# Optimization experiments

Hardware: AMD Instinct MI355X
Metric: run time of the kernel (lower is better)

Reference implementation:

```python
import jax, jax.numpy as jnp
import numpy as np
import math

DIM = 256

def setup_inputs() -> dict:
    key = jax.random.key(0)
    k1, k2, k3, k4, k5 = jax.random.split(key, 5)
    B, C, H, W = 4, DIM, 64, 64
    x = jax.random.normal(k1, (B, C, H, W), dtype=jnp.float32)
    fg_mask = jax.random.randint(k2, (B, 1, H, W), 0, 2, dtype=jnp.int32)
    s = 1.0 / math.sqrt(C)
    W_qkv = jax.random.uniform(k3, (3 * C, C), minval=-s, maxval=s, dtype=jnp.float32)
    W_proj = jax.random.uniform(k4, (C, C), minval=-s, maxval=s, dtype=jnp.float32)
    b_proj = jax.random.uniform(k5, (C,), minval=-s, maxval=s, dtype=jnp.float32)
    return {"x": x, "fg_mask": fg_mask, "W_qkv": W_qkv, "W_proj": W_proj, "b_proj": b_proj}

def reference(x, fg_mask, W_qkv, W_proj, b_proj):
    B, C, H, W = x.shape
    N = H * W
    xf = x.reshape(B, C, N).transpose(0, 2, 1)              # [B, N, C]
    qkv = jnp.einsum('bnc,dc->bnd', xf, W_qkv)              # [B, N, 3C]
    q, k, v = jnp.split(qkv, 3, axis=-1)                    # each [B, N, C]
    attn = jnp.einsum('bnc,bmc->bnm', q, k) / math.sqrt(C)  # [B, N, N]
    fg = fg_mask.reshape(B, N)                               # keys mask
    attn = jnp.where(fg[:, None, :] != 0, attn, -jnp.inf)
    a = jax.nn.softmax(attn, axis=-1)
    out = jnp.einsum('bnm,bmc->bnc', a, v)                  # [B, N, C]
    out = out @ W_proj.T + b_proj                           # [B, N, C]
    return out.transpose(0, 2, 1).reshape(B, C, H, W)
```

## Files before the change

### kernel.cpp

```cpp
#include <hip/hip_runtime.h>
#include <hip/hip_bf16.h>

#define BATCH 4
#define CDIM  256
#define NTOK  4096
#define THREE (3*CDIM)
#define VROWS 272

typedef unsigned short u16;
typedef unsigned char u8;
typedef long i64;
typedef __attribute__((ext_vector_type(4))) float f32x4;
typedef __attribute__((ext_vector_type(8))) short bf16x8;
typedef __attribute__((ext_vector_type(4))) unsigned int u32x4;

#define AS1 __attribute__((address_space(1)))
#define AS3 __attribute__((address_space(3)))

__device__ __forceinline__ u16 f2bf(float x) {
  unsigned int u = __float_as_uint(x);
  unsigned int r = (u + 0x7fffu + ((u >> 16) & 1u)) >> 16;
  return (u16)r;
}
__device__ __forceinline__ float bf2f(u16 v) {
  return __uint_as_float(((unsigned int)v) << 16);
}
__device__ __forceinline__ u8 f2fp8(float x) {
  int r = __builtin_amdgcn_cvt_pk_fp8_f32(x, 0.0f, 0, false);
  return (u8)(r & 0xff);
}
__device__ __forceinline__ void gload_lds16(const void* g, void* l) {
  __builtin_amdgcn_global_load_lds((AS1 const void*)g, (AS3 void*)l, 16, 0, 0);
}

#define SC8 0.30028132f

__global__ void k_prep(const float* __restrict__ Wqkv, const float* __restrict__ Wproj,
                       const int* __restrict__ fg,
                       u16* __restrict__ wq, u16* __restrict__ wp,
                       u16* __restrict__ Vt) {
  int i = blockIdx.x * 256 + threadIdx.x;
  const int nq = THREE * CDIM;
  const int np = CDIM * CDIM;
  const int nf = BATCH * NTOK;
  if (i < nq) { wq[i] = f2bf(Wqkv[i]); return; }
  int j = i - nq;
  if (j < np) { wp[j] = f2bf(Wproj[j]); return; }
  int k = j - np;
  if (k < nf) {
    int b = k >> 12, key = k & (NTOK - 1);
    Vt[((size_t)b * VROWS + 256) * NTOK + key] = fg[k] ? 0x3F80 : 0;
  }
}

__global__ __launch_bounds__(256) void k_transpose(const float* __restrict__ x, u16* __restrict__ xbf) {
  __shared__ float Ts[64][66];
  int n0 = blockIdx.x * 64;
  int c0 = blockIdx.y * 64;
  int b  = blockIdx.z;
  int tid = threadIdx.x;
  const float* xp = x + (size_t)b * CDIM * NTOK;
  int g16 = tid >> 4;
  int l16 = tid & 15;
#pragma unroll
  for (int i = 0; i < 4; ++i) {
    int cl = i * 16 + g16;
    int n4 = l16 * 4;
    *(f32x4*)&Ts[cl][n4] = *(const f32x4*)(xp + (size_t)(c0 + cl) * NTOK + n0 + n4);
  }
  __syncthreads();
#pragma unroll
  for (int i = 0; i < 4; ++i) {
    int nl = i * 16 + g16;
    int c4 = l16 * 4;
    ushort4 o;
    o.x = f2bf(Ts[c4 + 0][nl]);
    o.y = f2bf(Ts[c4 + 1][nl]);
    o.z = f2bf(Ts[c4 + 2][nl]);
    o.w = f2bf(Ts[c4 + 3][nl]);
    *(ushort4*)&xbf[((size_t)b * NTOK + n0 + nl) * CDIM + c0 + c4] = o;
  }
}

__global__ __launch_bounds__(256) void k_qkv(const u16* __restrict__ xbf, const u16* __restrict__ wq,
                                             const int* __restrict__ fg,
                                             u8* __restrict__ Qm8, u8* __restrict__ Km8,
                                             u16* __restrict__ Vt) {
  __shared__ u16 Al[128 * 64];
  __shared__ u16 Bl[128 * 64];
  int n0 = blockIdx.x * 128;
  int d0 = blockIdx.y * 128;
  int b  = blockIdx.z;
  int tid = threadIdx.x;
  int lane = tid & 63, w = tid >> 6;
  int lo = lane & 15, hi = lane >> 4;
  int wm = w >> 1, wn = w & 1;
  f32x4 acc[4][4] = {};
  const u16* Ab = xbf + ((size_t)b * NTOK + n0) * CDIM;
  const u16* Bb = wq + (size_t)d0 * CDIM;
  for (int kc = 0; kc < 256; kc += 64) {
    __syncthreads();
#pragma unroll
    for (int j = 0; j < 4; ++j) {
      int id = (j * 4 + w) * 64 + lane;
      int row = id >> 3, c = id & 7;
      int sc = c ^ (row & 7);
      gload_lds16(Ab + (size_t)row * CDIM + kc + sc * 8, &Al[(size_t)id * 8]);
      gload_lds16(Bb + (size_t)row * CDIM + kc + sc * 8, &Bl[(size_t)id * 8]);
    }
    __syncthreads();
#pragma unroll
    for (int kk = 0; kk < 2; ++kk) {
      bf16x8 af[4], bfr[4];
#pragma unroll
      for (int mi = 0; mi < 4; ++mi) {
        int row = wm * 64 + mi * 16 + lo;
        af[mi] = *(const bf16x8*)&Al[row * 64 + (((kk * 4 + hi) ^ (row & 7)) * 8)];
      }
#pragma unroll
      for (int ni = 0; ni < 4; ++ni) {
        int row = wn * 64 + ni * 16 + lo;
        bfr[ni] = *(const bf16x8*)&Bl[row * 64 + (((kk * 4 + hi) ^ (row & 7)) * 8)];
      }
#pragma unroll
      for (int mi = 0; mi < 4; ++mi)
#pragma unroll
        for (int ni = 0; ni < 4; ++ni)
          acc[mi][ni] = __builtin_amdgcn_mfma_f32_16x16x32_bf16(af[mi], bfr[ni], acc[mi][ni], 0, 0, 0);
    }
  }
  int seg = d0 >> 8;
#pragma unroll
  for (int mi = 0; mi < 4; ++mi) {
    int nbase = n0 + wm * 64 + mi * 16 + hi * 4;
#pragma unroll
    for (int ni = 0; ni < 4; ++ni) {
      int d = d0 + wn * 64 + ni * 16 + lo;
      if (seg == 0) {
#pragma unroll
        for (int r = 0; r < 4; ++r)
          Qm8[((size_t)b * NTOK + nbase + r) * CDIM + d] = f2fp8(acc[mi][ni][r] * SC8);
      } else if (seg == 1) {
        int dk = d - 256;
#pragma unroll
        for (int r = 0; r < 4; ++r)
          Km8[((size_t)b * NTOK + nbase + r) * CDIM + dk] = f2fp8(acc[mi][ni][r] * SC8);
      } else {
        int dv = d - 512;
        ushort4 pk;
        pk.x = fg[b * NTOK + nbase + 0] ? f2bf(acc[mi][ni][0]) : (u16)0;
        pk.y = fg[b * NTOK + nbase + 1] ? f2bf(acc[mi][ni][1]) : (u16)0;
        pk.z = fg[b * NTOK + nbase + 2] ? f2bf(acc[mi][ni][2]) : (u16)0;
        pk.w = fg[b * NTOK + nbase + 3] ? f2bf(acc[mi][ni][3]) : (u16)0;
        *(ushort4*)&Vt[((size_t)b * VROWS + dv) * NTOK + nbase] = pk;
      }
    }
  }
}

__global__ __launch_bounds__(256, 2) void k_attn(const u8* __restrict__ Qm8, const u8* __restrict__ Km8,
                                                 const u16* __restrict__ Vt,
                                                 u16* __restrict__ pacc, float2* __restrict__ pml,
                                                 int lsplit) {
  __shared__ u8  Kl[2][32 * 256];
  __shared__ u16 Vl[2][256 * 32];
  __shared__ u16 fgl[1024];
  const float FM = 12.0f;
  int nwg = gridDim.x;
  int cpx = nwg >> 3;
  int orig = blockIdx.x;
  int wg = (orig & 7) * cpx + (orig >> 3);
  int qt = wg & 31;
  int bs = wg >> 5;
  int s_k = bs & ((1 << lsplit) - 1);
  int b   = bs >> lsplit;
  int chunk = NTOK >> lsplit;
  int koff  = s_k * chunk;
  int iters = chunk >> 5;

  int tid = threadIdx.x;
  int lane = tid & 63, w = tid >> 6;
  int lo = lane & 15, hi = lane >> 4;
  int n0 = qt * 128 + w * 32;
  i64 qf[2][8];
#pragma unroll
  for (int s = 0; s < 2; ++s) {
    const u8* qp = Qm8 + ((size_t)b * NTOK + n0 + s * 16 + lo) * CDIM + hi * 8;
#pragma unroll
    for (int ks = 0; ks < 8; ++ks) qf[s][ks] = *(const i64*)(qp + ks * 32);
  }
  f32x4 acc[2][16] = {};
  float lsum[2] = {0.0f, 0.0f};
  const u8*  kbase = Km8 + (size_t)b * NTOK * CDIM;
  const u16* vbase = Vt + (size_t)b * VROWS * NTOK;
  const u16* fgrow = vbase + (size_t)256 * NTOK;
  int vr  = lane >> 2;
  int vc  = lane & 3;
  int srcA = lo + ((hi & 1) << 5);
  int srcB = srcA + 16;

  auto stage = [&](int buf, int m0) {
#pragma unroll
    for (int j = 0; j < 2; ++j) {
      int rl = w * 8 + j * 4 + (lane >> 4);
      int sb = ((lane & 15) << 4) ^ ((rl & 7) << 4);
      gload_lds16(kbase + (size_t)(m0 + rl) * CDIM + sb,
                  &Kl[buf][w * 2048 + j * 1024]);
    }
#pragma unroll
    for (int j = 0; j < 4; ++j) {
      int idx = j * 4 + w;
      int r = idx * 16 + vr;
      int d = vc ^ (r & 3) ^ ((r >> 2) & 3);
      gload_lds16(vbase + (size_t)r * NTOK + m0 + d * 8, &Vl[buf][idx * 512]);
    }
  };

  if (w < 2) gload_lds16(fgrow + koff + w * 512 + lane * 8, &fgl[w * 512 + lane * 8]);
  stage(0, koff);
  __syncthreads();
  for (int it = 0; it < iters; ++it) {
    int cur = it & 1;
    int m0 = koff + it * 32;
    if (it + 1 < iters) stage(cur ^ 1, m0 + 32);
    f32x4 sv[2][2];
#pragma unroll
    for (int s = 0; s < 2; ++s)
#pragma unroll
      for (int ni = 0; ni < 2; ++ni)
#pragma unroll
        for (int r = 0; r < 4; ++r) sv[s][ni][r] = -FM;
    __builtin_amdgcn_s_setprio(1);
#pragma unroll
    for (int ks = 0; ks < 8; ++ks) {
      i64 kf[2];
#pragma unroll
      for (int ni = 0; ni < 2; ++ni) {
        int row = ni * 16 + lo;
        int byteoff = row * 256 + ((((ks * 2 + (hi >> 1)) << 4) ^ ((row & 7) << 4))) + ((hi & 1) << 3);
        kf[ni] = *(const i64*)((const char*)&Kl[cur][0] + byteoff);
      }
#pragma unroll
      for (int s = 0; s < 2; ++s)
#pragma unroll
        for (int ni = 0; ni < 2; ++ni)
          sv[s][ni] = __builtin_amdgcn_mfma_f32_16x16x32_fp8_fp8(kf[ni], qf[s][ks], sv[s][ni], 0, 0, 0);
    }
    __builtin_amdgcn_s_setprio(0);
    float p0[2][2][4];
#pragma unroll
    for (int ni = 0; ni < 2; ++ni) {
      ushort4 fgu = *(const ushort4*)&fgl[it * 32 + ni * 16 + hi * 4];
      float fg0 = bf2f(fgu.x), fg1 = bf2f(fgu.y), fg2 = bf2f(fgu.z), fg3 = bf2f(fgu.w);
#pragma unroll
      for (int s = 0; s < 2; ++s) {
        float e0 = exp2f(sv[s][ni][0]);
        float e1 = exp2f(sv[s][ni][1]);
        float e2 = exp2f(sv[s][ni][2]);
        float e3 = exp2f(sv[s][ni][3]);
        lsum[s] += e0 * fg0 + e1 * fg1 + e2 * fg2 + e3 * fg3;
        p0[s][ni][0] = e0; p0[s][ni][1] = e1; p0[s][ni][2] = e2; p0[s][ni][3] = e3;
      }
    }
    bf16x8 pbf[2];
#pragma unroll
    for (int s = 0; s < 2; ++s) {
      unsigned int pk00, pk01, pk10, pk11;
      asm("v_cvt_pk_bf16_f32 %0, %1, %2" : "=v"(pk00) : "v"(p0[s][0][0]), "v"(p0[s][0][1]));
      asm("v_cvt_pk_bf16_f32 %0, %1, %2" : "=v"(pk01) : "v"(p0[s][0][2]), "v"(p0[s][0][3]));
      asm("v_cvt_pk_bf16_f32 %0, %1, %2" : "=v"(pk10) : "v"(p0[s][1][0]), "v"(p0[s][1][1]));
      asm("v_cvt_pk_bf16_f32 %0, %1, %2" : "=v"(pk11) : "v"(p0[s][1][2]), "v"(p0[s][1][3]));
      int a00 = __shfl((int)pk00, srcA); int a10 = __shfl((int)pk10, srcA);
      int a01 = __shfl((int)pk01, srcA); int a11 = __shfl((int)pk11, srcA);
      int b00 = __shfl((int)pk00, srcB); int b10 = __shfl((int)pk10, srcB);
      int b01 = __shfl((int)pk01, srcB); int b11 = __shfl((int)pk11, srcB);
      u32x4 tv;
      tv.x = (unsigned)(hi < 2 ? a00 : a10);
      tv.y = (unsigned)(hi < 2 ? a01 : a11);
      tv.z = (unsigned)(hi < 2 ? b00 : b10);
      tv.w = (unsigned)(hi < 2 ? b01 : b11);
      pbf[s] = __builtin_bit_cast(bf16x8, tv);
    }
    __builtin_amdgcn_s_setprio(1);
#pragma unroll
    for (int cf = 0; cf < 16; ++cf) {
      int row = cf * 16 + lo;
      const char* vp = (const char*)&Vl[cur][0] + row * 64 + ((hi ^ (lo & 3) ^ ((lo >> 2) & 3)) << 4);
      bf16x8 vb = *(const bf16x8*)vp;
#pragma unroll
      for (int s = 0; s < 2; ++s)
        acc[s][cf] = __builtin_amdgcn_mfma_f32_16x16x32_bf16(vb, pbf[s], acc[s][cf], 0, 0, 0);
    }
    __builtin_amdgcn_s_setprio(0);
    __syncthreads();
  }
  float ls[2];
#pragma unroll
  for (int s = 0; s < 2; ++s) {
    float t = lsum[s];
    t += __shfl_xor(t, 16);
    t += __shfl_xor(t, 32);
    ls[s] = t;
  }
  u16* pb = pacc + (((size_t)s_k * BATCH + b) * NTOK + n0) * CDIM;
  float2* pm = pml + ((size_t)s_k * BATCH + b) * NTOK + n0;
#pragma unroll
  for (int s = 0; s < 2; ++s) {
#pragma unroll
    for (int cf = 0; cf < 16; ++cf) {
      ushort4 st;
      st.x = f2bf(acc[s][cf][0]);
      st.y = f2bf(acc[s][cf][1]);
      st.z = f2bf(acc[s][cf][2]);
      st.w = f2bf(acc[s][cf][3]);
      *(ushort4*)&pb[(size_t)(s * 16 + lo) * CDIM + cf * 16 + hi * 4] = st;
    }
    if (lane < 16) {
      float2 v; v.x = FM; v.y = ls[s];
      pm[s * 16 + lane] = v;
    }
  }
}

__global__ __launch_bounds__(256) void k_proj(const u16* __restrict__ pacc,
                                              const float2* __restrict__ pml,
                                              const u16* __restrict__ wp,
                                              const float* __restrict__ bproj, float* __restrict__ out) {
  __shared__ u16 Al[128 * 64];
  __shared__ u16 Bl[128][72];
  __shared__ float invl[128];
  const size_t RN = (size_t)BATCH * NTOK;
  int n0 = blockIdx.x * 128;
  int c0 = blockIdx.y * 128;
  int b  = blockIdx.z;
  int tid = threadIdx.x;
  int lane = tid & 63, w = tid >> 6;
  int lo = lane & 15, hi = lane >> 4;
  int wm = w >> 1, wn = w & 1;
  if (tid < 128) {
    float d = 0.0f;
#pragma unroll
    for (int s = 0; s < 4; ++s)
      d += pml[(size_t)s * RN + (size_t)b * NTOK + n0 + tid].y;
    invl[tid] = 1.0f / d;
  }
  f32x4 acc[4][4] = {};
  const u16* Ab = wp + (size_t)c0 * CDIM;
  for (int kcs = 0; kcs < 256; kcs += 64) {
    __syncthreads();
#pragma unroll
    for (int j = 0; j < 4; ++j) {
      int id = (j * 4 + w) * 64 + lane;
      int row = id >> 3, c = id & 7;
      int sc = c ^ (row & 7);
      gload_lds16(Ab + (size_t)row * CDIM + kcs + sc * 8, &Al[(size_t)id * 8]);
    }
#pragma unroll
    for (int i = 0; i < 4; ++i) {
      int cid = i * 256 + tid;
      int row = cid >> 3, cc = cid & 7;
      size_t off = ((size_t)b * NTOK + n0 + row) * CDIM + kcs + cc * 8;
      float v[8] = {0, 0, 0, 0, 0, 0, 0, 0};
#pragma unroll
      for (int s = 0; s < 4; ++s) {
        uint4 u = *(const uint4*)(pacc + (size_t)s * RN * CDIM + off);
        const u16* pu = (const u16*)&u;
#pragma unroll
        for (int j = 0; j < 8; ++j) v[j] += bf2f(pu[j]);
      }
      float iv = invl[row];
      ushort4 o0, o1;
      o0.x = f2bf(v[0] * iv); o0.y = f2bf(v[1] * iv); o0.z = f2bf(v[2] * iv); o0.w = f2bf(v[3] * iv);
      o1.x = f2bf(v[4] * iv); o1.y = f2bf(v[5] * iv); o1.z = f2bf(v[6] * iv); o1.w = f2bf(v[7] * iv);
      *(ushort4*)&Bl[row][cc * 8]     = o0;
      *(ushort4*)&Bl[row][cc * 8 + 4] = o1;
    }
    __syncthreads();
#pragma unroll
    for (int kk = 0; kk < 2; ++kk) {
      bf16x8 af[4], bfr[4];
#pragma unroll
      for (int mi = 0; mi < 4; ++mi) {
        int row = wm * 64 + mi * 16 + lo;
        af[mi] = *(const bf16x8*)&Al[row * 64 + (((kk * 4 + hi) ^ (row & 7)) * 8)];
      }
#pragma unroll
      for (int ni = 0; ni < 4; ++ni) bfr[ni] = *(const bf16x8*)&Bl[wn * 64 + ni * 16 + lo][kk * 32 + hi * 8];
#pragma unroll
      for (int mi = 0; mi < 4; ++mi)
#pragma unroll
        for (int ni = 0; ni < 4; ++ni)
          acc[mi][ni] = __builtin_amdgcn_mfma_f32_16x16x32_bf16(af[mi], bfr[ni], acc[mi][ni], 0, 0, 0);
    }
  }
#pragma unroll
  for (int mi = 0; mi < 4; ++mi) {
    int cbase = c0 + wm * 64 + mi * 16 + hi * 4;
#pragma unroll
    for (int r = 0; r < 4; ++r) {
      float bias = bproj[cbase + r];
#pragma unroll
      for (int ni = 0; ni < 4; ++ni) {
        int n = n0 + wn * 64 + ni * 16 + lo;
        out[((size_t)b * CDIM + cbase + r) * NTOK + n] = acc[mi][ni][r] + bias;
      }
    }
  }
}

extern "C" void kernel_launch(void* const* d_in, const int* in_sizes, int n_in,
                              void* d_out, int out_size, void* d_ws, size_t ws_size,
                              hipStream_t stream) {
  const float* x     = (const float*)d_in[0];
  const int*   fg    = (const int*)d_in[1];
  const float* Wqkv  = (const float*)d_in[2];
  const float* Wproj = (const float*)d_in[3];
  const float* bproj = (const float*)d_in[4];
  float* out = (float*)d_out;
  char* ws = (char*)d_ws;
  u16*   xbf  = (u16*)(ws);
  u8*    Qm8  = (u8*)(ws + 8388608);
  u8*    Km8  = (u8*)(ws + 12582912);
  u16*   Vt   = (u16*)(ws + 16777216);
  u16*   wq   = (u16*)(ws + 25690112);
  u16*   wp   = (u16*)(ws + 26083328);
  u16*   pacc = (u16*)(ws + 26214400);
  float2* pml = (float2*)(ws + 59768832);

  k_prep<<<1088, 256, 0, stream>>>(Wqkv, Wproj, fg, wq, wp, Vt);
  k_transpose<<<dim3(64, 4, 4), 256, 0, stream>>>(x, xbf);
  k_qkv<<<dim3(32, 6, 4), 256, 0, stream>>>(xbf, wq, fg, Qm8, Km8, Vt);
  k_attn<<<512, 256, 0, stream>>>(Qm8, Km8, Vt, pacc, pml, 2);
  k_proj<<<dim3(32, 2, 4), 256, 0, stream>>>(pacc, pml, wp, bproj, out);
}
```

Before: 138.6 us.

## Halve attention query tile per wave to double workgroups and raise occupancy

Each wave in the attention kernel now handles 16 query rows instead of 32, so a workgroup covers 64 queries and the grid doubles to 1024 workgroups. Launch bounds go to 3 waves per SIMD, which fits because the accumulator register footprint is halved. The goal is more parallelism and better latency hiding across CUs. In exchange, every K/V tile staged into LDS is reused by half as many queries, so K/V traffic and LDS staging per unit of work double.

```diff
diff --git a/kernel.cpp b/kernel.cpp
--- a/kernel.cpp
+++ b/kernel.cpp
@@ -158,7 +158,7 @@
   }
 }
 
-__global__ __launch_bounds__(256, 2) void k_attn(const u8* __restrict__ Qm8, const u8* __restrict__ Km8,
+__global__ __launch_bounds__(256, 3) void k_attn(const u8* __restrict__ Qm8, const u8* __restrict__ Km8,
                                                  const u16* __restrict__ Vt,
                                                  u16* __restrict__ pacc, float2* __restrict__ pml,
                                                  int lsplit) {
@@ -170,8 +170,8 @@
   int cpx = nwg >> 3;
   int orig = blockIdx.x;
   int wg = (orig & 7) * cpx + (orig >> 3);
-  int qt = wg & 31;
-  int bs = wg >> 5;
+  int qt = wg & 63;
+  int bs = wg >> 6;
   int s_k = bs & ((1 << lsplit) - 1);
   int b   = bs >> lsplit;
   int chunk = NTOK >> lsplit;
@@ -181,16 +181,13 @@
   int tid = threadIdx.x;
   int lane = tid & 63, w = tid >> 6;
   int lo = lane & 15, hi = lane >> 4;
-  int n0 = qt * 128 + w * 32;
-  i64 qf[2][8];
-#pragma unroll
-  for (int s = 0; s < 2; ++s) {
-    const u8* qp = Qm8 + ((size_t)b * NTOK + n0 + s * 16 + lo) * CDIM + hi * 8;
-#pragma unroll
-    for (int ks = 0; ks < 8; ++ks) qf[s][ks] = *(const i64*)(qp + ks * 32);
-  }
-  f32x4 acc[2][16] = {};
-  float lsum[2] = {0.0f, 0.0f};
+  int n0 = qt * 64 + w * 16;
+  i64 qf[8];
+  const u8* qp = Qm8 + ((size_t)b * NTOK + n0 + lo) * CDIM + hi * 8;
+#pragma unroll
+  for (int ks = 0; ks < 8; ++ks) qf[ks] = *(const i64*)(qp + ks * 32);
+  f32x4 acc[16] = {};
+  float lsum = 0.0f;
   const u8*  kbase = Km8 + (size_t)b * NTOK * CDIM;
   const u16* vbase = Vt + (size_t)b * VROWS * NTOK;
   const u16* fgrow = vbase + (size_t)256 * NTOK;
@@ -223,13 +220,11 @@
     int cur = it & 1;
     int m0 = koff + it * 32;
     if (it + 1 < iters) stage(cur ^ 1, m0 + 32);
-    f32x4 sv[2][2];
-#pragma unroll
-    for (int s = 0; s < 2; ++s)
-#pragma unroll
-      for (int ni = 0; ni < 2; ++ni)
-#pragma unroll
-        for (int r = 0; r < 4; ++r) sv[s][ni][r] = -FM;
+    f32x4 sv[2];
+#pragma unroll
+    for (int ni = 0; ni < 2; ++ni)
+#pragma unroll
+      for (int r = 0; r < 4; ++r) sv[ni][r] = -FM;
     __builtin_amdgcn_s_setprio(1);
 #pragma unroll
     for (int ks = 0; ks < 8; ++ks) {
@@ -241,35 +236,28 @@
         kf[ni] = *(const i64*)((const char*)&Kl[cur][0] + byteoff);
       }
 #pragma unroll
-      for (int s = 0; s < 2; ++s)
-#pragma unroll
-        for (int ni = 0; ni < 2; ++ni)
-          sv[s][ni] = __builtin_amdgcn_mfma_f32_16x16x32_fp8_fp8(kf[ni], qf[s][ks], sv[s][ni], 0, 0, 0);
+      for (int ni = 0; ni < 2; ++ni)
+        sv[ni] = __builtin_amdgcn_mfma_f32_16x16x32_fp8_fp8(kf[ni], qf[ks], sv[ni], 0, 0, 0);
     }
     __builtin_amdgcn_s_setprio(0);
-    float p0[2][2][4];
+    float p0[2][4];
 #pragma unroll
     for (int ni = 0; ni < 2; ++ni) {
       ushort4 fgu = *(const ushort4*)&fgl[it * 32 + ni * 16 + hi * 4];
-      float fg0 = bf2f(fgu.x), fg1 = bf2f(fgu.y), fg2 = bf2f(fgu.z), fg3 = bf2f(fgu.w);
-#pragma unroll
-      for (int s = 0; s < 2; ++s) {
-        float e0 = exp2f(sv[s][ni][0]);
-        float e1 = exp2f(sv[s][ni][1]);
-        float e2 = exp2f(sv[s][ni][2]);
-        float e3 = exp2f(sv[s][ni][3]);
-        lsum[s] += e0 * fg0 + e1 * fg1 + e2 * fg2 + e3 * fg3;
-        p0[s][ni][0] = e0; p0[s][ni][1] = e1; p0[s][ni][2] = e2; p0[s][ni][3] = e3;
-      }
-    }
-    bf16x8 pbf[2];
-#pragma unroll
-    for (int s = 0; s < 2; ++s) {
+      float e0 = exp2f(sv[ni][0]);
+      float e1 = exp2f(sv[ni][1]);
+      float e2 = exp2f(sv[ni][2]);
+      float e3 = exp2f(sv[ni][3]);
+      lsum += e0 * bf2f(fgu.x) + e1 * bf2f(fgu.y) + e2 * bf2f(fgu.z) + e3 * bf2f(fgu.w);
+      p0[ni][0] = e0; p0[ni][1] = e1; p0[ni][2] = e2; p0[ni][3] = e3;
+    }
+    bf16x8 pbf;
+    {
       unsigned int pk00, pk01, pk10, pk11;
-      asm("v_cvt_pk_bf16_f32 %0, %1, %2" : "=v"(pk00) : "v"(p0[s][0][0]), "v"(p0[s][0][1]));
-      asm("v_cvt_pk_bf16_f32 %0, %1, %2" : "=v"(pk01) : "v"(p0[s][0][2]), "v"(p0[s][0][3]));
-      asm("v_cvt_pk_bf16_f32 %0, %1, %2" : "=v"(pk10) : "v"(p0[s][1][0]), "v"(p0[s][1][1]));
-      asm("v_cvt_pk_bf16_f32 %0, %1, %2" : "=v"(pk11) : "v"(p0[s][1][2]), "v"(p0[s][1][3]));
+      asm("v_cvt_pk_bf16_f32 %0, %1, %2" : "=v"(pk00) : "v"(p0[0][0]), "v"(p0[0][1]));
+      asm("v_cvt_pk_bf16_f32 %0, %1, %2" : "=v"(pk01) : "v"(p0[0][2]), "v"(p0[0][3]));
+      asm("v_cvt_pk_bf16_f32 %0, %1, %2" : "=v"(pk10) : "v"(p0[1][0]), "v"(p0[1][1]));
+      asm("v_cvt_pk_bf16_f32 %0, %1, %2" : "=v"(pk11) : "v"(p0[1][2]), "v"(p0[1][3]));
       int a00 = __shfl((int)pk00, srcA); int a10 = __shfl((int)pk10, srcA);
       int a01 = __shfl((int)pk01, srcA); int a11 = __shfl((int)pk11, srcA);
       int b00 = __shfl((int)pk00, srcB); int b10 = __shfl((int)pk10, srcB);
@@ -279,7 +267,7 @@
       tv.y = (unsigned)(hi < 2 ? a01 : a11);
       tv.z = (unsigned)(hi < 2 ? b00 : b10);
       tv.w = (unsigned)(hi < 2 ? b01 : b11);
-      pbf[s] = __builtin_bit_cast(bf16x8, tv);
+      pbf = __builtin_bit_cast(bf16x8, tv);
     }
     __builtin_amdgcn_s_setprio(1);
 #pragma unroll
@@ -287,38 +275,32 @@
       int row = cf * 16 + lo;
       const char* vp = (const char*)&Vl[cur][0] + row * 64 + ((hi ^ (lo & 3) ^ ((lo >> 2) & 3)) << 4);
       bf16x8 vb = *(const bf16x8*)vp;
-#pragma unroll
-      for (int s = 0; s < 2; ++s)
-        acc[s][cf] = __builtin_amdgcn_mfma_f32_16x16x32_bf16(vb, pbf[s], acc[s][cf], 0, 0, 0);
+      acc[cf] = __builtin_amdgcn_mfma_f32_16x16x32_bf16(vb, pbf, acc[cf], 0, 0, 0);
     }
     __builtin_amdgcn_s_setprio(0);
     __syncthreads();
   }
-  float ls[2];
-#pragma unroll
-  for (int s = 0; s < 2; ++s) {
-    float t = lsum[s];
+  float ls;
+  {
+    float t = lsum;
     t += __shfl_xor(t, 16);
     t += __shfl_xor(t, 32);
-    ls[s] = t;
+    ls = t;
   }
   u16* pb = pacc + (((size_t)s_k * BATCH + b) * NTOK + n0) * CDIM;
   float2* pm = pml + ((size_t)s_k * BATCH + b) * NTOK + n0;
 #pragma unroll
-  for (int s = 0; s < 2; ++s) {
-#pragma unroll
-    for (int cf = 0; cf < 16; ++cf) {
-      ushort4 st;
-      st.x = f2bf(acc[s][cf][0]);
-      st.y = f2bf(acc[s][cf][1]);
-      st.z = f2bf(acc[s][cf][2]);
-      st.w = f2bf(acc[s][cf][3]);
-      *(ushort4*)&pb[(size_t)(s * 16 + lo) * CDIM + cf * 16 + hi * 4] = st;
-    }
-    if (lane < 16) {
-      float2 v; v.x = FM; v.y = ls[s];
-      pm[s * 16 + lane] = v;
-    }
+  for (int cf = 0; cf < 16; ++cf) {
+    ushort4 st;
+    st.x = f2bf(acc[cf][0]);
+    st.y = f2bf(acc[cf][1]);
+    st.z = f2bf(acc[cf][2]);
+    st.w = f2bf(acc[cf][3]);
+    *(ushort4*)&pb[(size_t)lo * CDIM + cf * 16 + hi * 4] = st;
+  }
+  if (lane < 16) {
+    float2 v; v.x = FM; v.y = ls;
+    pm[lane] = v;
   }
 }
 
@@ -430,6 +412,6 @@
   k_prep<<<1088, 256, 0, stream>>>(Wqkv, Wproj, fg, wq, wp, Vt);
   k_transpose<<<dim3(64, 4, 4), 256, 0, stream>>>(x, xbf);
   k_qkv<<<dim3(32, 6, 4), 256, 0, stream>>>(xbf, wq, fg, Qm8, Km8, Vt);
-  k_attn<<<512, 256, 0, stream>>>(Qm8, Km8, Vt, pacc, pml, 2);
+  k_attn<<<1024, 256, 0, stream>>>(Qm8, Km8, Vt, pacc, pml, 2);
   k_proj<<<dim3(32, 2, 4), 256, 0, stream>>>(pacc, pml, wp, bproj, out);
 }
```

After: 178.4 us. +28.8%, slower.
